# Kernel optimization log

Hardware: AMD Instinct MI355X
Metric: run time of the kernel (lower is better)

The kernel has to match this reference:

```python
import jax, jax.numpy as jnp
import numpy as np

GRID_SIZE, K, NUM_EXPERTS = 5, 3, 8
N_MLP, N_KAN = 4, 4
B, D, H, O = 4096, 512, 2048, 512


def _bspline_basis(x, grid, k):
    """Cox-de Boor recursion, vectorized. x: [B, D]; grid: [G]. Returns [B, D, G-k-1]."""
    xe = x[..., None]
    # order-0: indicator of grid interval
    b = ((grid[:-1] <= xe) & (xe < grid[1:])).astype(x.dtype)  # [B, D, G-1]
    for kk in range(1, k + 1):
        t_i = grid[: -(kk + 1)]
        t_ik = grid[kk:-1]
        t_ik1 = grid[kk + 1:]
        t_i1 = grid[1:-kk]
        left = (xe - t_i) / (t_ik - t_i) * b[..., :-1]
        right = (t_ik1 - xe) / (t_ik1 - t_i1) * b[..., 1:]
        b = left + right
    return b


def setup_inputs() -> dict:
    key = jax.random.key(0)
    ks = jax.random.split(key, 8)
    x = jax.random.normal(ks[0], (B, D), dtype=jnp.float32)
    # Router output: binary expert mask; rows with no active group fall back to expert 7
    mask = (jax.random.uniform(ks[1], (B, NUM_EXPERTS)) < 0.3).astype(jnp.float32)
    other = jnp.zeros((NUM_EXPERTS,), jnp.float32).at[7].set(1.0)
    expert_mask = jnp.where(mask.sum(axis=1, keepdims=True) == 0, other[None, :], mask)
    s_d = 1.0 / np.sqrt(D)
    s_h = 1.0 / np.sqrt(H)
    gate_w = jax.random.normal(ks[2], (D, NUM_EXPERTS), jnp.float32) * s_d
    gate_b = jnp.zeros((NUM_EXPERTS,), jnp.float32)
    mlp_w1 = jax.random.normal(ks[3], (N_MLP, D, H), jnp.float32) * s_d
    mlp_b1 = jnp.zeros((N_MLP, H), jnp.float32)
    mlp_w2 = jax.random.normal(ks[4], (N_MLP, H, O), jnp.float32) * s_h
    mlp_b2 = jnp.zeros((N_MLP, O), jnp.float32)
    kan_scaling = jnp.ones((N_KAN, D, O), jnp.float32)
    kan_coeff = jax.random.normal(ks[5], (N_KAN, D, O, GRID_SIZE + K), jnp.float32)
    return dict(x=x, expert_mask=expert_mask, gate_w=gate_w, gate_b=gate_b,
                mlp_w1=mlp_w1, mlp_b1=mlp_b1, mlp_w2=mlp_w2, mlp_b2=mlp_b2,
                kan_scaling=kan_scaling, kan_coeff=kan_coeff)


def reference(x, expert_mask, gate_w, gate_b, mlp_w1, mlp_b1, mlp_w2, mlp_b2,
              kan_scaling, kan_coeff):
    # gate softmax + router mask + renormalize
    gate = jax.nn.softmax(x @ gate_w + gate_b, axis=1)          # [B, E]
    masked = gate * expert_mask
    w = masked / (masked.sum(axis=1, keepdims=True) + 1e-9)      # [B, E]

    # MLP experts (eval mode -> dropout is identity)
    h = jax.nn.relu(jnp.einsum('bd,edh->ebh', x, mlp_w1) + mlp_b1[:, None, :])
    mlp_out = jnp.einsum('ebh,eho->ebo', h, mlp_w2) + mlp_b2[:, None, :]  # [4, B, O]

    # KAN experts: uniform grid extended by k knots each side (spacing 2/grid_size)
    hg = 2.0 / GRID_SIZE
    grid = jnp.arange(GRID_SIZE + 2 * K + 1, dtype=x.dtype) * hg - (1.0 + K * hg)
    basis = _bspline_basis(x, grid, K)                           # [B, D, 8]
    ceff = kan_coeff * kan_scaling[..., None]                    # [4, D, O, 8]
    kan_out = jnp.einsum('big,eiog->ebo', basis, ceff)           # [4, B, O]

    expert_outputs = jnp.concatenate([mlp_out, kan_out], axis=0)  # [8, B, O]
    out = jnp.einsum('ebo,be->bo', expert_outputs, w)             # [B, O]
    return out, expert_mask, w
```

## Files before the change

kernel.cpp:

```cpp
#include <hip/hip_runtime.h>

typedef __attribute__((ext_vector_type(4))) float f32x4;
typedef __attribute__((ext_vector_type(8))) __bf16 bf16x8;
typedef __attribute__((ext_vector_type(4))) unsigned short u16x4;
typedef __attribute__((ext_vector_type(8))) unsigned short u16x8;

#define NB 4096
#define ND 512
#define NH 2048
#define NO 512

__device__ __forceinline__ unsigned short f2bf(float f) {
  unsigned int u = __float_as_uint(f);
  u += 0x7fffu + ((u >> 16) & 1u);
  return (unsigned short)(u >> 16);
}
__device__ __forceinline__ float bf2f(unsigned short u) {
  return __uint_as_float(((unsigned int)u) << 16);
}
__device__ __forceinline__ void gload_lds16(const void* g, void* l) {
  __builtin_amdgcn_global_load_lds(
      (const __attribute__((address_space(1))) unsigned int*)g,
      (__attribute__((address_space(3))) unsigned int*)l, 16, 0, 0);
}

__global__ void gate_kernel(const float* __restrict__ x, const float* __restrict__ emask,
                            const float* __restrict__ gw, const float* __restrict__ gb,
                            float* __restrict__ w_out, float* __restrict__ mask_out) {
  int b = blockIdx.x;
  int lane = threadIdx.x;
  float l8[8] = {0,0,0,0,0,0,0,0};
  const float* xr = x + (size_t)b * ND;
  for (int d = lane; d < ND; d += 64) {
    float xv = xr[d];
    const float* g = gw + d * 8;
#pragma unroll
    for (int e = 0; e < 8; ++e) l8[e] = fmaf(xv, g[e], l8[e]);
  }
#pragma unroll
  for (int off = 32; off > 0; off >>= 1) {
#pragma unroll
    for (int e = 0; e < 8; ++e) l8[e] += __shfl_xor(l8[e], off);
  }
  float m = -1e30f;
#pragma unroll
  for (int e = 0; e < 8; ++e) { l8[e] += gb[e]; m = fmaxf(m, l8[e]); }
  float s = 0.f, p[8];
#pragma unroll
  for (int e = 0; e < 8; ++e) { p[e] = expf(l8[e] - m); s += p[e]; }
  float inv = 1.f / s;
  float mk[8], me[8], ms = 0.f;
#pragma unroll
  for (int e = 0; e < 8; ++e) {
    mk[e] = emask[(size_t)b * 8 + e];
    me[e] = p[e] * inv * mk[e];
    ms += me[e];
  }
  float winv = 1.f / (ms + 1e-9f);
  if (lane == 0) {
#pragma unroll
    for (int e = 0; e < 8; ++e) {
      w_out[(size_t)b * 8 + e] = me[e] * winv;
      mask_out[(size_t)b * 8 + e] = mk[e];
    }
  }
}

__global__ void cast_x_kernel(const float* __restrict__ x, unsigned short* __restrict__ xb) {
  size_t i = ((size_t)blockIdx.x * 256 + threadIdx.x) * 4;
  f32x4 v = *(const f32x4*)(x + i);
  u16x4 r;
#pragma unroll
  for (int j = 0; j < 4; ++j) r[j] = f2bf(v[j]);
  *(u16x4*)(xb + i) = r;
}

__global__ void basis_kernel(const float* __restrict__ x, unsigned short* __restrict__ bas) {
  size_t t = (size_t)blockIdx.x * 256 + threadIdx.x;
  float xv = x[t];
  const float hg = 0.4f;
  float tt[12];
#pragma unroll
  for (int j = 0; j < 12; ++j) tt[j] = -2.2f + hg * (float)j;
  float b0[11];
#pragma unroll
  for (int j = 0; j < 11; ++j) b0[j] = (tt[j] <= xv && xv < tt[j + 1]) ? 1.f : 0.f;
  float b1[10], b2[9], b3[8];
#pragma unroll
  for (int j = 0; j < 10; ++j) b1[j] = ((xv - tt[j]) * b0[j] + (tt[j + 2] - xv) * b0[j + 1]) * (1.f / (1.f * hg));
#pragma unroll
  for (int j = 0; j < 9; ++j)  b2[j] = ((xv - tt[j]) * b1[j] + (tt[j + 3] - xv) * b1[j + 1]) * (1.f / (2.f * hg));
#pragma unroll
  for (int j = 0; j < 8; ++j)  b3[j] = ((xv - tt[j]) * b2[j] + (tt[j + 4] - xv) * b2[j + 1]) * (1.f / (3.f * hg));
  u16x8 r;
#pragma unroll
  for (int j = 0; j < 8; ++j) r[j] = f2bf(b3[j]);
  *(u16x8*)(bas + t * 8) = r;
}

__global__ void transpose_cast(const float* __restrict__ in, unsigned short* __restrict__ outp,
                               int R, int Cc) {
  __shared__ float tile[32][33];
  int e = blockIdx.z;
  int c0 = blockIdx.x * 32, r0 = blockIdx.y * 32;
  int tx = threadIdx.x & 31, ty = threadIdx.x >> 5;
  const float* ine = in + (size_t)e * R * Cc;
  unsigned short* oute = outp + (size_t)e * R * Cc;
#pragma unroll
  for (int j = 0; j < 32; j += 8)
    tile[ty + j][tx] = ine[(size_t)(r0 + ty + j) * Cc + (c0 + tx)];
  __syncthreads();
#pragma unroll
  for (int j = 0; j < 32; j += 8)
    oute[(size_t)(c0 + ty + j) * R + (r0 + tx)] = f2bf(tile[tx][ty + j]);
}

__global__ void make_cefft(const float* __restrict__ coeff, const float* __restrict__ scal,
                           unsigned short* __restrict__ outp) {
  size_t t = (size_t)blockIdx.x * 256 + threadIdx.x;
  int i = (int)(t & 511);
  int o = (int)((t >> 9) & 511);
  int e = (int)(t >> 18);
  size_t io = ((size_t)e * 512 + i) * 512 + o;
  const f32x4* cp = (const f32x4*)(coeff + io * 8);
  f32x4 c0 = cp[0], c1 = cp[1];
  float s = scal[io];
  u16x8 r;
#pragma unroll
  for (int j = 0; j < 4; ++j) r[j] = f2bf(c0[j] * s);
#pragma unroll
  for (int j = 0; j < 4; ++j) r[4 + j] = f2bf(c1[j] * s);
  *(u16x8*)(outp + ((size_t)e * 512 + o) * 4096 + (size_t)i * 8) = r;
}

template <int MODE, int ZSPLIT>
__global__ __launch_bounds__(512, 2) void gemm_bt(
    const unsigned short* __restrict__ A, size_t strideAe, int lda,
    const unsigned short* __restrict__ Bm, size_t strideBe, int ldb,
    const float* __restrict__ bias, int strideBiasE,
    unsigned short* __restrict__ C, size_t strideCe, size_t strideHalf, int ldc,
    int Kspan, int zshift, int gx) {
  __shared__ __align__(16) char lsA[3 * 16384];
  __shared__ __align__(16) char lsB[3 * 16384];
  const int tid = threadIdx.x;
  const int lane = tid & 63, wid = tid >> 6;
  const int wr = wid >> 2, wc = wid & 3;
  const int wg = blockIdx.x;
  const int xcd = wg & 7, u = wg >> 3;
  const int z = xcd / ZSPLIT;
  const int gxp = gx / ZSPLIT;
  const int bx = (xcd % ZSPLIT) * gxp + (u % gxp);
  const int by = u / gxp;
  const int brow = by * 256, bcol = bx * 256;
  const int e = z >> zshift;
  const int half = z & ((1 << zshift) - 1);
  const unsigned short* Ae = A + (size_t)e * strideAe + (size_t)half * Kspan;
  const unsigned short* Be = Bm + (size_t)e * strideBe + (size_t)half * Kspan;
  const int NT = Kspan >> 5;

  const int fr = lane & 15, fc = lane >> 4;
  const int sR = tid >> 2, ssc = tid & 3;

  auto stage = [&](int buf, int t2) {
#pragma unroll
    for (int q = 0; q < 2; ++q) {
      int R = q * 128 + sR;
      int kk = t2 * 32 + ((ssc ^ ((R >> 1) & 3)) << 3);
      gload_lds16(Ae + (size_t)(brow + R) * lda + (size_t)kk,
                  lsA + buf * 16384 + q * 8192 + tid * 16);
    }
#pragma unroll
    for (int q = 0; q < 2; ++q) {
      int R = q * 128 + sR;
      int kk = t2 * 32 + ((ssc ^ ((R >> 1) & 3)) << 3);
      gload_lds16(Be + (size_t)(bcol + R) * ldb + (size_t)kk,
                  lsB + buf * 16384 + q * 8192 + tid * 16);
    }
  };

  f32x4 acc[8][4] = {};

  stage(0, 0);
  stage(1, 1);
  asm volatile("s_waitcnt vmcnt(4)" ::: "memory");
  __builtin_amdgcn_s_barrier();

  int bi = 0;
  for (int t = 0; t < NT; ++t) {
    const char* bA = lsA + bi * 16384;
    const char* bB = lsB + bi * 16384;
    const int pb = (bi == 0) ? 2 : bi - 1;
    const bool pf = (t + 2 < NT);

    bf16x8 af[8], bfrag[4];
#pragma unroll
    for (int i = 0; i < 8; ++i) {
      int ra = wr * 128 + i * 16 + fr;
      af[i] = *(const bf16x8*)(bA + ra * 64 + ((fc ^ ((ra >> 1) & 3)) << 4));
    }
#pragma unroll
    for (int n = 0; n < 4; ++n) {
      int rb = wc * 64 + n * 16 + fr;
      bfrag[n] = *(const bf16x8*)(bB + rb * 64 + ((fc ^ ((rb >> 1) & 3)) << 4));
    }
    if (pf) stage(pb, t + 2);
    __builtin_amdgcn_s_barrier();
    asm volatile("s_waitcnt lgkmcnt(0)" ::: "memory");
    __builtin_amdgcn_sched_barrier(0);
    __builtin_amdgcn_s_setprio(1);
#pragma unroll
    for (int mi = 0; mi < 8; ++mi)
#pragma unroll
      for (int ni = 0; ni < 4; ++ni)
        acc[mi][ni] = __builtin_amdgcn_mfma_f32_16x16x32_bf16(bfrag[ni], af[mi], acc[mi][ni], 0, 0, 0);
    __builtin_amdgcn_s_setprio(0);
    if (pf)               asm volatile("s_waitcnt vmcnt(4)" ::: "memory");
    else if (t + 1 < NT)  asm volatile("s_waitcnt vmcnt(0)" ::: "memory");
    __builtin_amdgcn_s_barrier();

    bi = (bi == 2) ? 0 : bi + 1;
  }

  unsigned short* Ce = C + (size_t)e * strideCe + (size_t)half * strideHalf;
#pragma unroll
  for (int mi = 0; mi < 8; ++mi) {
    int row = brow + wr * 128 + mi * 16 + fr;
#pragma unroll
    for (int ni = 0; ni < 4; ++ni) {
      int col0 = bcol + wc * 64 + ni * 16 + (fc << 2);
      u16x4 r;
      if constexpr (MODE == 0) {
        f32x4 bv = *(const f32x4*)(bias + e * strideBiasE + col0);
#pragma unroll
        for (int j = 0; j < 4; ++j) r[j] = f2bf(fmaxf(acc[mi][ni][j] + bv[j], 0.f));
      } else {
#pragma unroll
        for (int j = 0; j < 4; ++j) r[j] = f2bf(acc[mi][ni][j]);
      }
      *(u16x4*)(Ce + (size_t)row * ldc + col0) = r;
    }
  }
}

__global__ void combine_kernel(const unsigned short* __restrict__ eoM,
                               const unsigned short* __restrict__ eoK,
                               const float* __restrict__ b2,
                               const float* __restrict__ w, float* __restrict__ out) {
  int b = blockIdx.x;
  int o = threadIdx.x * 4;
  float wv[8];
#pragma unroll
  for (int e = 0; e < 8; ++e) wv[e] = w[(size_t)b * 8 + e];
  f32x4 acc = {0.f, 0.f, 0.f, 0.f};
#pragma unroll
  for (int e = 0; e < 4; ++e) {
    u16x4 m0 = *(const u16x4*)(eoM + ((size_t)e * NB + b) * NO + o);
    u16x4 m1 = *(const u16x4*)(eoM + ((size_t)(4 + e) * NB + b) * NO + o);
    f32x4 bb = *(const f32x4*)(b2 + e * NO + o);
#pragma unroll
    for (int j = 0; j < 4; ++j)
      acc[j] = fmaf(wv[e], bf2f(m0[j]) + bf2f(m1[j]) + bb[j], acc[j]);
  }
#pragma unroll
  for (int e = 0; e < 4; ++e) {
    u16x4 k0 = *(const u16x4*)(eoK + ((size_t)e * NB + b) * NO + o);
    u16x4 k1 = *(const u16x4*)(eoK + ((size_t)(4 + e) * NB + b) * NO + o);
#pragma unroll
    for (int j = 0; j < 4; ++j)
      acc[j] = fmaf(wv[4 + e], bf2f(k0[j]) + bf2f(k1[j]), acc[j]);
  }
  *(f32x4*)(out + (size_t)b * NO + o) = acc;
}

extern "C" void kernel_launch(void* const* d_in, const int* in_sizes, int n_in,
                              void* d_out, int out_size, void* d_ws, size_t ws_size,
                              hipStream_t stream) {
  (void)in_sizes; (void)n_in; (void)out_size; (void)ws_size;
  const float* x      = (const float*)d_in[0];
  const float* emask  = (const float*)d_in[1];
  const float* gate_w = (const float*)d_in[2];
  const float* gate_b = (const float*)d_in[3];
  const float* mlp_w1 = (const float*)d_in[4];
  const float* mlp_b1 = (const float*)d_in[5];
  const float* mlp_w2 = (const float*)d_in[6];
  const float* mlp_b2 = (const float*)d_in[7];
  const float* kan_s  = (const float*)d_in[8];
  const float* kan_c  = (const float*)d_in[9];

  float* out = (float*)d_out;
  float* mask_out = out + (size_t)NB * NO;
  float* w_out    = mask_out + (size_t)NB * 8;

  char* ws = (char*)d_ws;
  size_t off = 0;
  auto take = [&](size_t bytes) { size_t r = off; off += (bytes + 255) & ~(size_t)255; return r; };
  unsigned short* w1t   = (unsigned short*)(ws + take((size_t)4 * NH * ND * 2));
  unsigned short* w2t   = (unsigned short*)(ws + take((size_t)4 * NO * NH * 2));
  unsigned short* cefft = (unsigned short*)(ws + take((size_t)4 * NO * (ND * 8) * 2));
  unsigned short* xbf   = (unsigned short*)(ws + take((size_t)NB * ND * 2));
  unsigned short* eoM   = (unsigned short*)(ws + take((size_t)8 * NB * NO * 2));
  unsigned short* hbuf  = (unsigned short*)(ws + take((size_t)4 * NB * NH * 2));
  unsigned short* bas   = hbuf;
  unsigned short* eoK   = (unsigned short*)((char*)hbuf + (size_t)2 * NB * NH * 2);

  gate_kernel<<<NB, 64, 0, stream>>>(x, emask, gate_w, gate_b, w_out, mask_out);
  cast_x_kernel<<<(NB * ND) / (256 * 4), 256, 0, stream>>>(x, xbf);
  transpose_cast<<<dim3(NH / 32, ND / 32, 4), 256, 0, stream>>>(mlp_w1, w1t, ND, NH);
  transpose_cast<<<dim3(NO / 32, NH / 32, 4), 256, 0, stream>>>(mlp_w2, w2t, NH, NO);
  make_cefft<<<(4 * ND * NO) / 256, 256, 0, stream>>>(kan_c, kan_s, cefft);

  gemm_bt<0, 2><<<512, 512, 0, stream>>>(
      xbf, 0, ND,
      w1t, (size_t)NH * ND, ND,
      mlp_b1, NH,
      hbuf, (size_t)NB * NH, 0, NH, ND, 0, NH / 256);
  gemm_bt<2, 1><<<256, 512, 0, stream>>>(
      hbuf, (size_t)NB * NH, NH,
      w2t, (size_t)NO * NH, NH,
      nullptr, 0,
      eoM, (size_t)NB * NO, (size_t)4 * NB * NO, NO, NH / 2, 1, NO / 256);
  basis_kernel<<<(NB * ND) / 256, 256, 0, stream>>>(x, bas);
  gemm_bt<2, 1><<<256, 512, 0, stream>>>(
      bas, 0, ND * 8,
      cefft, (size_t)NO * (ND * 8), ND * 8,
      nullptr, 0,
      eoK, (size_t)NB * NO, (size_t)4 * NB * NO, NO, (ND * 8) / 2, 1, NO / 256);

  combine_kernel<<<NB, NO / 4, 0, stream>>>(eoM, eoK, mlp_b2, w_out, out);
}
```

Before: 237.6 us.

## Co-schedule MLP layer-1 GEMM and KAN GEMM in a single grouped launch

```diff
diff --git a/kernel.cpp b/kernel.cpp
--- a/kernel.cpp
+++ b/kernel.cpp
@@ -133,30 +133,35 @@
   *(u16x8*)(outp + ((size_t)e * 512 + o) * 4096 + (size_t)i * 8) = r;
 }
 
-template <int MODE, int ZSPLIT>
-__global__ __launch_bounds__(512, 2) void gemm_bt(
-    const unsigned short* __restrict__ A, size_t strideAe, int lda,
-    const unsigned short* __restrict__ Bm, size_t strideBe, int ldb,
-    const float* __restrict__ bias, int strideBiasE,
-    unsigned short* __restrict__ C, size_t strideCe, size_t strideHalf, int ldc,
-    int Kspan, int zshift, int gx) {
+struct GemmArgs {
+  const unsigned short* A; size_t sAe; int lda;
+  const unsigned short* B; size_t sBe; int ldb;
+  const float* bias; int sBias;
+  unsigned short* C; size_t sCe; size_t sHalf; int ldc;
+  int Kspan; int zshift; int gx; int nxy;
+  int mode;
+};
+
+__global__ __launch_bounds__(512, 2) void gemm_fused(int nL1, GemmArgs a1, GemmArgs a2) {
   __shared__ __align__(16) char lsA[3 * 16384];
   __shared__ __align__(16) char lsB[3 * 16384];
+  const int wg = blockIdx.x;
+  const GemmArgs g = (wg < nL1) ? a1 : a2;
+  const int wgl = (wg < nL1) ? wg : wg - nL1;
   const int tid = threadIdx.x;
   const int lane = tid & 63, wid = tid >> 6;
   const int wr = wid >> 2, wc = wid & 3;
-  const int wg = blockIdx.x;
-  const int xcd = wg & 7, u = wg >> 3;
-  const int z = xcd / ZSPLIT;
-  const int gxp = gx / ZSPLIT;
-  const int bx = (xcd % ZSPLIT) * gxp + (u % gxp);
-  const int by = u / gxp;
-  const int brow = by * 256, bcol = bx * 256;
-  const int e = z >> zshift;
-  const int half = z & ((1 << zshift) - 1);
-  const unsigned short* Ae = A + (size_t)e * strideAe + (size_t)half * Kspan;
-  const unsigned short* Be = Bm + (size_t)e * strideBe + (size_t)half * Kspan;
-  const int NT = Kspan >> 5;
+  const int z = wgl / g.nxy;
+  int rem = wgl % g.nxy;
+  rem = (rem & 7) * (g.nxy >> 3) + (rem >> 3);
+  const int bcol = (rem % g.gx) * 256;
+  const int brow = (rem / g.gx) * 256;
+  const int e = z >> g.zshift;
+  const int half = z & ((1 << g.zshift) - 1);
+  const unsigned short* Ae = g.A + (size_t)e * g.sAe + (size_t)half * g.Kspan;
+  const unsigned short* Be = g.B + (size_t)e * g.sBe + (size_t)half * g.Kspan;
+  const int lda = g.lda, ldb = g.ldb;
+  const int NT = g.Kspan >> 5;
 
   const int fr = lane & 15, fc = lane >> 4;
   const int sR = tid >> 2, ssc = tid & 3;
@@ -221,7 +226,8 @@
     bi = (bi == 2) ? 0 : bi + 1;
   }
 
-  unsigned short* Ce = C + (size_t)e * strideCe + (size_t)half * strideHalf;
+  unsigned short* Ce = g.C + (size_t)e * g.sCe + (size_t)half * g.sHalf;
+  const int ldc = g.ldc;
 #pragma unroll
   for (int mi = 0; mi < 8; ++mi) {
     int row = brow + wr * 128 + mi * 16 + fr;
@@ -229,8 +235,8 @@
     for (int ni = 0; ni < 4; ++ni) {
       int col0 = bcol + wc * 64 + ni * 16 + (fc << 2);
       u16x4 r;
-      if constexpr (MODE == 0) {
-        f32x4 bv = *(const f32x4*)(bias + e * strideBiasE + col0);
+      if (g.mode == 0) {
+        f32x4 bv = *(const f32x4*)(g.bias + e * g.sBias + col0);
 #pragma unroll
         for (int j = 0; j < 4; ++j) r[j] = f2bf(fmaxf(acc[mi][ni][j] + bv[j], 0.f));
       } else {
@@ -275,7 +281,7 @@
 extern "C" void kernel_launch(void* const* d_in, const int* in_sizes, int n_in,
                               void* d_out, int out_size, void* d_ws, size_t ws_size,
                               hipStream_t stream) {
-  (void)in_sizes; (void)n_in; (void)out_size; (void)ws_size;
+  (void)in_sizes; (void)n_in; (void)out_size;
   const float* x      = (const float*)d_in[0];
   const float* emask  = (const float*)d_in[1];
   const float* gate_w = (const float*)d_in[2];
@@ -298,10 +304,20 @@
   unsigned short* w2t   = (unsigned short*)(ws + take((size_t)4 * NO * NH * 2));
   unsigned short* cefft = (unsigned short*)(ws + take((size_t)4 * NO * (ND * 8) * 2));
   unsigned short* xbf   = (unsigned short*)(ws + take((size_t)NB * ND * 2));
-  unsigned short* eoM   = (unsigned short*)(ws + take((size_t)8 * NB * NO * 2));
+  unsigned short* regA  = (unsigned short*)(ws + take((size_t)8 * NB * NO * 2));
   unsigned short* hbuf  = (unsigned short*)(ws + take((size_t)4 * NB * NH * 2));
-  unsigned short* bas   = hbuf;
-  unsigned short* eoK   = (unsigned short*)((char*)hbuf + (size_t)2 * NB * NH * 2);
+  size_t base_need = off;
+  size_t eoK_off = base_need;
+  const bool fused = (ws_size >= base_need + (size_t)8 * NB * NO * 2);
+  unsigned short* eoM = regA;
+  unsigned short* bas, *eoK;
+  if (fused) {
+    bas = regA;
+    eoK = (unsigned short*)(ws + eoK_off);
+  } else {
+    bas = hbuf;
+    eoK = (unsigned short*)((char*)hbuf + (size_t)2 * NB * NH * 2);
+  }
 
   gate_kernel<<<NB, 64, 0, stream>>>(x, emask, gate_w, gate_b, w_out, mask_out);
   cast_x_kernel<<<(NB * ND) / (256 * 4), 256, 0, stream>>>(x, xbf);
@@ -309,22 +325,32 @@
   transpose_cast<<<dim3(NO / 32, NH / 32, 4), 256, 0, stream>>>(mlp_w2, w2t, NH, NO);
   make_cefft<<<(4 * ND * NO) / 256, 256, 0, stream>>>(kan_c, kan_s, cefft);
 
-  gemm_bt<0, 2><<<512, 512, 0, stream>>>(
-      xbf, 0, ND,
-      w1t, (size_t)NH * ND, ND,
-      mlp_b1, NH,
-      hbuf, (size_t)NB * NH, 0, NH, ND, 0, NH / 256);
-  gemm_bt<2, 1><<<256, 512, 0, stream>>>(
-      hbuf, (size_t)NB * NH, NH,
-      w2t, (size_t)NO * NH, NH,
-      nullptr, 0,
-      eoM, (size_t)NB * NO, (size_t)4 * NB * NO, NO, NH / 2, 1, NO / 256);
-  basis_kernel<<<(NB * ND) / 256, 256, 0, stream>>>(x, bas);
-  gemm_bt<2, 1><<<256, 512, 0, stream>>>(
-      bas, 0, ND * 8,
-      cefft, (size_t)NO * (ND * 8), ND * 8,
-      nullptr, 0,
-      eoK, (size_t)NB * NO, (size_t)4 * NB * NO, NO, (ND * 8) / 2, 1, NO / 256);
+  GemmArgs aL1 = { xbf, 0, ND,
+                   w1t, (size_t)NH * ND, ND,
+                   mlp_b1, NH,
+                   hbuf, (size_t)NB * NH, 0, NH,
+                   ND, 0, NH / 256, (NH / 256) * (NB / 256), 0 };
+  GemmArgs aL2 = { hbuf, (size_t)NB * NH, NH,
+                   w2t, (size_t)NO * NH, NH,
+                   nullptr, 0,
+                   eoM, (size_t)NB * NO, (size_t)4 * NB * NO, NO,
+                   NH / 2, 1, NO / 256, (NO / 256) * (NB / 256), 2 };
+  GemmArgs aL3 = { bas, 0, ND * 8,
+                   cefft, (size_t)NO * (ND * 8), ND * 8,
+                   nullptr, 0,
+                   eoK, (size_t)NB * NO, (size_t)4 * NB * NO, NO,
+                   (ND * 8) / 2, 1, NO / 256, (NO / 256) * (NB / 256), 2 };
+
+  if (fused) {
+    basis_kernel<<<(NB * ND) / 256, 256, 0, stream>>>(x, bas);
+    gemm_fused<<<512 + 256, 512, 0, stream>>>(512, aL1, aL3);
+    gemm_fused<<<256, 512, 0, stream>>>(0, aL2, aL2);
+  } else {
+    gemm_fused<<<512, 512, 0, stream>>>(512, aL1, aL1);
+    gemm_fused<<<256, 512, 0, stream>>>(0, aL2, aL2);
+    basis_kernel<<<(NB * ND) / 256, 256, 0, stream>>>(x, bas);
+    gemm_fused<<<256, 512, 0, stream>>>(0, aL3, aL3);
+  }
 
   combine_kernel<<<NB, NO / 4, 0, stream>>>(eoM, eoK, mlp_b2, w_out, out);
 }
```

Measured after the change: 233.0 us. About the same (-1.9%).
